# Kernel optimization log

Hardware: AMD Instinct MI355X
Metric: run time of the kernel (lower is better)

The kernel has to match this reference:

```python
import jax, jax.numpy as jnp
import numpy as np

N = 65536          # nodes
E = 1048576        # edges (avg degree 16)
K = 5              # B-spline kernel size per dim (dim=3 -> 125 kernels)
F_IN, F_OUT = 1, 32
GRID = 32          # first sparse_voxel_max_pool: size = 1/32 -> 32^3 voxels
NUM_VOX = GRID ** 3

# enumerate the 2^3 corners of the degree-1 B-spline support
_BITS = np.array([[(b >> d) & 1 for d in range(3)] for b in range(8)], dtype=np.int32)  # [8,3]
_STRIDES = np.array([1, K, K * K], dtype=np.int32)  # kernel index strides per dim


def setup_inputs() -> dict:
    key = jax.random.key(0)
    ks = jax.random.split(key, 7)
    x = jax.random.normal(ks[0], (N, F_IN), dtype=jnp.float32)
    edge_index = jax.random.randint(ks[1], (2, E), 0, N, dtype=jnp.int32)
    pseudo = jax.random.uniform(ks[2], (E, 3), dtype=jnp.float32)   # edge pseudo-coords in [0,1]^3
    pos = jax.random.uniform(ks[3], (N, 3), dtype=jnp.float32)      # node positions in [0,1]^3
    W = jax.random.normal(ks[4], (K ** 3, F_IN, F_OUT), dtype=jnp.float32) * 0.1
    W_root = jax.random.normal(ks[5], (F_IN, F_OUT), dtype=jnp.float32) * 0.1
    bias = jax.random.normal(ks[6], (F_OUT,), dtype=jnp.float32) * 0.1
    return {"x": x, "edge_index": edge_index, "pseudo": pseudo, "pos": pos,
            "W": W, "W_root": W_root, "bias": bias}


def spline_basis(pseudo):
    """Degree-1 open B-spline basis. Returns (weights [E,8], kernel_idx [E,8])."""
    v = pseudo * (K - 1)                                   # [E,3] in [0, K-1]
    i0 = jnp.clip(jnp.floor(v), 0, K - 2)                  # lower knot per dim
    f = v - i0                                             # fractional part
    i0 = i0.astype(jnp.int32)
    bits = jnp.asarray(_BITS)                              # [8,3]
    idx = i0[:, None, :] + bits[None]                      # [E,8,3]
    w = jnp.where(bits[None].astype(bool), f[:, None, :], 1.0 - f[:, None, :])
    B = w.prod(axis=-1)                                    # [E,8]
    kidx = (idx * jnp.asarray(_STRIDES)).sum(axis=-1)      # [E,8] in [0,125)
    return B, kidx


def spline_conv(x, edge_index, pseudo, W, W_root, bias):
    src, dst = edge_index[0], edge_index[1]
    B, kidx = spline_basis(pseudo)                         # [E,8], [E,8]
    xj = x[src]                                            # [E,F_IN] edge-wise gather
    Wg = W[kidx]                                           # [E,8,F_IN,F_OUT]
    msg = jnp.einsum('es,ef,esfo->eo', B, xj, Wg)          # basis-weighted messages [E,F_OUT]
    agg = jax.ops.segment_sum(msg, dst, num_segments=N)    # scatter-add
    deg = jax.ops.segment_sum(jnp.ones((E,), jnp.float32), dst, num_segments=N)
    out = agg / jnp.clip(deg, 1.0)[:, None] + x @ W_root + bias  # mean aggr + root + bias
    return out


def reference(x, edge_index, pseudo, pos, W, W_root, bias):
    h = jax.nn.elu(spline_conv(x, edge_index, pseudo, W, W_root, bias))  # [N,32]
    # sparse voxel max pooling: hash positions to a 32^3 grid, scatter-max features
    vid = jnp.clip(jnp.floor(pos * GRID), 0, GRID - 1).astype(jnp.int32)  # [N,3]
    vidx = vid[:, 0] + GRID * vid[:, 1] + GRID * GRID * vid[:, 2]         # [N]
    pooled = jax.ops.segment_max(h, vidx, num_segments=NUM_VOX)           # [32768,32]
    pooled = jnp.where(jnp.isfinite(pooled), pooled, 0.0)                 # empty voxels -> 0
    return pooled
```

## Files before the change

kernel.cpp:

```cpp
#include <hip/hip_runtime.h>
#include <math.h>

#define F_OUT     32
#define GRID_DIM  32
#define NUM_VOX   (GRID_DIM * GRID_DIM * GRID_DIM)

#define NPB   64
#define NBKT  1024
#define SEB   1024
#define CAP   1344
#define SCS   132
#define DEGS  125

__device__ __forceinline__ unsigned int enc_f32(float f) {
    unsigned int u = __float_as_uint(f);
    return (u & 0x80000000u) ? ~u : (u | 0x80000000u);
}
__device__ __forceinline__ float dec_f32(unsigned int e) {
    return (e & 0x80000000u) ? __uint_as_float(e ^ 0x80000000u)
                             : __uint_as_float(~e);
}

__global__ __launch_bounds__(512) void scatter_kernel(
    const int*   __restrict__ src,
    const int*   __restrict__ dst,
    const float* __restrict__ x,
    const float* __restrict__ pseudo,
    float4* __restrict__ payload,
    unsigned int* __restrict__ cursor,
    int E)
{
    __shared__ unsigned int sHist[NBKT];
    __shared__ unsigned int sCur[NBKT];

    const int t  = threadIdx.x;
    const int e0 = blockIdx.x * SEB;

    for (int i = t; i < NBKT; i += 512) sHist[i] = 0;
    __syncthreads();

    unsigned short dloc[SEB / 512];
    float4 pay[SEB / 512];
    #pragma unroll
    for (int i = 0; i < SEB / 512; ++i) {
        int e = e0 + i * 512 + t;
        if (e < E) {
            int d = dst[e];
            int s = src[e];
            float p0 = pseudo[3 * e], p1 = pseudo[3 * e + 1], p2 = pseudo[3 * e + 2];
            float xj = x[s];
            unsigned int q2 = (unsigned int)(p2 * 65535.0f + 0.5f) & 0xFFFFu;
            unsigned int w  = q2 | ((unsigned int)(d & 63) << 16);
            dloc[i] = (unsigned short)d;
            pay[i]  = make_float4(p0, p1, xj, __uint_as_float(w));
            atomicAdd(&sHist[d >> 6], 1u);
        }
    }
    __syncthreads();

    for (int b = t; b < NBKT; b += 512) {
        unsigned int c = sHist[b];
        sCur[b] = c ? atomicAdd(&cursor[b], c) : 0u;
    }
    __syncthreads();

    #pragma unroll
    for (int i = 0; i < SEB / 512; ++i) {
        int e = e0 + i * 512 + t;
        if (e < E) {
            unsigned int bkt  = (unsigned int)dloc[i] >> 6;
            unsigned int slot = atomicAdd(&sCur[bkt], 1u);
            if (slot < CAP)
                payload[(size_t)bkt * CAP + slot] = pay[i];
        }
    }
}

__device__ __forceinline__ void process_edge(float4 r, float* sC)
{
    float xj = r.z;
    unsigned int w = __float_as_uint(r.w);
    int   rel = (int)((w >> 16) & 63u);
    float p2  = (float)(w & 0xFFFFu) * (1.0f / 65535.0f);

    float v0 = r.x * 4.0f, v1 = r.y * 4.0f, v2 = p2 * 4.0f;
    float i0 = fminf(fmaxf(floorf(v0), 0.0f), 3.0f);
    float i1 = fminf(fmaxf(floorf(v1), 0.0f), 3.0f);
    float i2 = fminf(fmaxf(floorf(v2), 0.0f), 3.0f);
    float f0 = v0 - i0, f1 = v1 - i1, f2 = v2 - i2;
    float g0 = 1.0f - f0, g1 = 1.0f - f1, g2 = 1.0f - f2;
    int k = (int)i0 + 5 * (int)i1 + 25 * (int)i2;

    float w00 = g0 * g1, w10 = f0 * g1, w01 = g0 * f1, w11 = f0 * f1;
    float a2 = xj * g2, b2 = xj * f2;
    float* row = sC + rel * SCS;
    atomicAdd(row + k +  0, w00 * a2);
    atomicAdd(row + k +  1, w10 * a2);
    atomicAdd(row + k +  5, w01 * a2);
    atomicAdd(row + k +  6, w11 * a2);
    atomicAdd(row + k + 25, w00 * b2);
    atomicAdd(row + k + 26, w10 * b2);
    atomicAdd(row + k + 30, w01 * b2);
    atomicAdd(row + k + 31, w11 * b2);
    atomicAdd(row + DEGS, 1.0f);
}

__global__ __launch_bounds__(512) void owner_kernel(
    const float4* __restrict__ payload,
    const unsigned int* __restrict__ cursor,
    const float* __restrict__ W,
    const float* __restrict__ x,
    const float* __restrict__ W_root,
    const float* __restrict__ bias,
    const float* __restrict__ pos,
    unsigned int* __restrict__ pooled,
    int Nn)
{
    __shared__ __align__(16) float sC[NPB * SCS];

    const int t = threadIdx.x;
    const int b = blockIdx.x;

    for (int i = t; i < NPB * SCS / 4; i += 512)
        *(float4*)&sC[i * 4] = make_float4(0.f, 0.f, 0.f, 0.f);
    __syncthreads();

    int cnt = (int)cursor[b];
    if (cnt > CAP) cnt = CAP;
    const float4* slab = payload + (size_t)b * CAP;
    {
        int i = t;
        if (i < cnt) {
            float4 r = slab[i];
            for (i += 512; i < cnt; i += 512) {
                float4 rn = slab[i];
                process_edge(r, sC);
                r = rn;
            }
            process_edge(r, sC);
        }
    }
    __syncthreads();

    const int node = t & 63;
    const int cg   = t >> 6;
    const float* crow = sC + node * SCS;
    float4 acc = make_float4(0.f, 0.f, 0.f, 0.f);
    #pragma unroll 8
    for (int k4 = 0; k4 < 31; ++k4) {
        float4 r = *(const float4*)&crow[k4 * 4];
        const float* wp = W + (k4 * 4) * F_OUT + cg * 4;
        float4 w0 = *(const float4*)(wp);
        float4 w1 = *(const float4*)(wp + F_OUT);
        float4 w2 = *(const float4*)(wp + 2 * F_OUT);
        float4 w3 = *(const float4*)(wp + 3 * F_OUT);
        acc.x += r.x * w0.x + r.y * w1.x + r.z * w2.x + r.w * w3.x;
        acc.y += r.x * w0.y + r.y * w1.y + r.z * w2.y + r.w * w3.y;
        acc.z += r.x * w0.z + r.y * w1.z + r.z * w2.z + r.w * w3.z;
        acc.w += r.x * w0.w + r.y * w1.w + r.z * w2.w + r.w * w3.w;
    }
    {
        float r = crow[124];
        const float* wp = W + 124 * F_OUT + cg * 4;
        acc.x += r * wp[0]; acc.y += r * wp[1];
        acc.z += r * wp[2]; acc.w += r * wp[3];
    }
    float dg = fmaxf(crow[DEGS], 1.0f);
    int   n  = b * NPB + node;
    float xn = (n < Nn) ? x[n] : 0.0f;
    float4 wr = *(const float4*)(W_root + cg * 4);
    float4 bs = *(const float4*)(bias + cg * 4);
    __syncthreads();

    if (n < Nn) {
        float h;
        h = acc.x / dg + xn * wr.x + bs.x; h = h > 0.f ? h : expm1f(h); sC[node * SCS + cg * 4 + 0] = h;
        h = acc.y / dg + xn * wr.y + bs.y; h = h > 0.f ? h : expm1f(h); sC[node * SCS + cg * 4 + 1] = h;
        h = acc.z / dg + xn * wr.z + bs.z; h = h > 0.f ? h : expm1f(h); sC[node * SCS + cg * 4 + 2] = h;
        h = acc.w / dg + xn * wr.w + bs.w; h = h > 0.f ? h : expm1f(h); sC[node * SCS + cg * 4 + 3] = h;
    }
    __syncthreads();

    for (int item = t; item < NPB * F_OUT; item += 512) {
        int nr = item >> 5, o = item & 31;
        int nn = b * NPB + nr;
        if (nn >= Nn) break;
        int vx = min(max((int)floorf(pos[3 * nn + 0] * (float)GRID_DIM), 0), GRID_DIM - 1);
        int vy = min(max((int)floorf(pos[3 * nn + 1] * (float)GRID_DIM), 0), GRID_DIM - 1);
        int vz = min(max((int)floorf(pos[3 * nn + 2] * (float)GRID_DIM), 0), GRID_DIM - 1);
        int vidx = vx + GRID_DIM * vy + GRID_DIM * GRID_DIM * vz;
        atomicMax(&pooled[(size_t)vidx * F_OUT + o], enc_f32(sC[nr * SCS + o]));
    }
}

__global__ __launch_bounds__(256) void finalize_kernel(
    const unsigned int* pooled,
    float* out, int M)
{
    int i = blockIdx.x * blockDim.x + threadIdx.x;
    if (i >= M) return;
    unsigned int u = pooled[i];
    out[i] = (u == 0u) ? 0.0f : dec_f32(u);
}

extern "C" void kernel_launch(void* const* d_in, const int* in_sizes, int n_in,
                              void* d_out, int out_size, void* d_ws, size_t ws_size,
                              hipStream_t stream) {
    const float* x       = (const float*)d_in[0];
    const int*   ei      = (const int*)  d_in[1];
    const float* pseudo  = (const float*)d_in[2];
    const float* pos     = (const float*)d_in[3];
    const float* W       = (const float*)d_in[4];
    const float* W_root  = (const float*)d_in[5];
    const float* bias    = (const float*)d_in[6];

    const int E   = in_sizes[1] / 2;
    const int Nn  = in_sizes[0];
    const int nSB = (E + SEB - 1) / SEB;
    const int nb  = (Nn + NPB - 1) / NPB;

    float4*       payload = (float4*)d_ws;
    unsigned int* cursor  = (unsigned int*)((char*)d_ws + (size_t)NBKT * CAP * sizeof(float4));

    unsigned int* pooled = (unsigned int*)d_out;
    const int M = (out_size < NUM_VOX * F_OUT) ? out_size : NUM_VOX * F_OUT;

    hipMemsetAsync(cursor, 0, NBKT * sizeof(unsigned int), stream);
    hipMemsetAsync(d_out, 0, (size_t)M * sizeof(float), stream);

    scatter_kernel<<<nSB, 512, 0, stream>>>(ei, ei + E, x, pseudo, payload, cursor, E);
    owner_kernel<<<nb, 512, 0, stream>>>(payload, cursor, W, x, W_root, bias, pos,
                                         pooled, Nn);
    finalize_kernel<<<(M + 255) / 256, 256, 0, stream>>>(pooled, (float*)d_out, M);
}
```

Before: 179.7 us.

## Split owner blocks into node halves and pad bucket cursors to separate lines

Each 64-node bucket is now handled by two 256-thread blocks, each owning 32 nodes. Each block reads the whole bucket slab and discards edges whose destination falls in the other half. This doubles the block count and halves the shared accumulator per block, which is meant to raise occupancy and parallelism. The cost is that every payload slab is read twice from global memory. Bucket cursors are also spaced 32 words apart so the global atomics in the scatter kernel do not contend on the same cache lines.

```diff
diff --git a/kernel.cpp b/kernel.cpp
--- a/kernel.cpp
+++ b/kernel.cpp
@@ -11,6 +11,7 @@
 #define CAP   1344
 #define SCS   132
 #define DEGS  125
+#define CSTR  32
 
 __device__ __forceinline__ unsigned int enc_f32(float f) {
     unsigned int u = __float_as_uint(f);
@@ -60,7 +61,7 @@
 
     for (int b = t; b < NBKT; b += 512) {
         unsigned int c = sHist[b];
-        sCur[b] = c ? atomicAdd(&cursor[b], c) : 0u;
+        sCur[b] = c ? atomicAdd(&cursor[(size_t)b * CSTR], c) : 0u;
     }
     __syncthreads();
 
@@ -76,12 +77,14 @@
     }
 }
 
-__device__ __forceinline__ void process_edge(float4 r, float* sC)
-{
+__device__ __forceinline__ void process_edge(float4 r, float* sC, int half)
+{
+    unsigned int w = __float_as_uint(r.w);
+    int rel6 = (int)((w >> 16) & 63u);
+    if ((rel6 >> 5) != half) return;
+
     float xj = r.z;
-    unsigned int w = __float_as_uint(r.w);
-    int   rel = (int)((w >> 16) & 63u);
-    float p2  = (float)(w & 0xFFFFu) * (1.0f / 65535.0f);
+    float p2 = (float)(w & 0xFFFFu) * (1.0f / 65535.0f);
 
     float v0 = r.x * 4.0f, v1 = r.y * 4.0f, v2 = p2 * 4.0f;
     float i0 = fminf(fmaxf(floorf(v0), 0.0f), 3.0f);
@@ -93,7 +96,7 @@
 
     float w00 = g0 * g1, w10 = f0 * g1, w01 = g0 * f1, w11 = f0 * f1;
     float a2 = xj * g2, b2 = xj * f2;
-    float* row = sC + rel * SCS;
+    float* row = sC + (rel6 & 31) * SCS;
     atomicAdd(row + k +  0, w00 * a2);
     atomicAdd(row + k +  1, w10 * a2);
     atomicAdd(row + k +  5, w01 * a2);
@@ -105,7 +108,7 @@
     atomicAdd(row + DEGS, 1.0f);
 }
 
-__global__ __launch_bounds__(512) void owner_kernel(
+__global__ __launch_bounds__(256) void owner_kernel(
     const float4* __restrict__ payload,
     const unsigned int* __restrict__ cursor,
     const float* __restrict__ W,
@@ -116,34 +119,36 @@
     unsigned int* __restrict__ pooled,
     int Nn)
 {
-    __shared__ __align__(16) float sC[NPB * SCS];
-
-    const int t = threadIdx.x;
-    const int b = blockIdx.x;
-
-    for (int i = t; i < NPB * SCS / 4; i += 512)
+    __shared__ __align__(16) float sC[32 * SCS];
+
+    const int t    = threadIdx.x;
+    const int bp   = blockIdx.x;
+    const int b    = bp >> 1;
+    const int half = bp & 1;
+
+    for (int i = t; i < 32 * SCS / 4; i += 256)
         *(float4*)&sC[i * 4] = make_float4(0.f, 0.f, 0.f, 0.f);
     __syncthreads();
 
-    int cnt = (int)cursor[b];
+    int cnt = (int)cursor[(size_t)b * CSTR];
     if (cnt > CAP) cnt = CAP;
     const float4* slab = payload + (size_t)b * CAP;
     {
         int i = t;
         if (i < cnt) {
             float4 r = slab[i];
-            for (i += 512; i < cnt; i += 512) {
+            for (i += 256; i < cnt; i += 256) {
                 float4 rn = slab[i];
-                process_edge(r, sC);
+                process_edge(r, sC, half);
                 r = rn;
             }
-            process_edge(r, sC);
+            process_edge(r, sC, half);
         }
     }
     __syncthreads();
 
-    const int node = t & 63;
-    const int cg   = t >> 6;
+    const int node = t & 31;
+    const int cg   = t >> 5;
     const float* crow = sC + node * SCS;
     float4 acc = make_float4(0.f, 0.f, 0.f, 0.f);
     #pragma unroll 8
@@ -166,7 +171,7 @@
         acc.z += r * wp[2]; acc.w += r * wp[3];
     }
     float dg = fmaxf(crow[DEGS], 1.0f);
-    int   n  = b * NPB + node;
+    int   n  = b * NPB + half * 32 + node;
     float xn = (n < Nn) ? x[n] : 0.0f;
     float4 wr = *(const float4*)(W_root + cg * 4);
     float4 bs = *(const float4*)(bias + cg * 4);
@@ -181,9 +186,9 @@
     }
     __syncthreads();
 
-    for (int item = t; item < NPB * F_OUT; item += 512) {
+    for (int item = t; item < 32 * F_OUT; item += 256) {
         int nr = item >> 5, o = item & 31;
-        int nn = b * NPB + nr;
+        int nn = b * NPB + half * 32 + nr;
         if (nn >= Nn) break;
         int vx = min(max((int)floorf(pos[3 * nn + 0] * (float)GRID_DIM), 0), GRID_DIM - 1);
         int vy = min(max((int)floorf(pos[3 * nn + 1] * (float)GRID_DIM), 0), GRID_DIM - 1);
@@ -217,7 +222,7 @@
     const int E   = in_sizes[1] / 2;
     const int Nn  = in_sizes[0];
     const int nSB = (E + SEB - 1) / SEB;
-    const int nb  = (Nn + NPB - 1) / NPB;
+    const int nb  = 2 * ((Nn + NPB - 1) / NPB);
 
     float4*       payload = (float4*)d_ws;
     unsigned int* cursor  = (unsigned int*)((char*)d_ws + (size_t)NBKT * CAP * sizeof(float4));
@@ -225,11 +230,11 @@
     unsigned int* pooled = (unsigned int*)d_out;
     const int M = (out_size < NUM_VOX * F_OUT) ? out_size : NUM_VOX * F_OUT;
 
-    hipMemsetAsync(cursor, 0, NBKT * sizeof(unsigned int), stream);
+    hipMemsetAsync(cursor, 0, (size_t)NBKT * CSTR * sizeof(unsigned int), stream);
     hipMemsetAsync(d_out, 0, (size_t)M * sizeof(float), stream);
 
     scatter_kernel<<<nSB, 512, 0, stream>>>(ei, ei + E, x, pseudo, payload, cursor, E);
-    owner_kernel<<<nb, 512, 0, stream>>>(payload, cursor, W, x, W_root, bias, pos,
+    owner_kernel<<<nb, 256, 0, stream>>>(payload, cursor, W, x, W_root, bias, pos,
                                          pooled, Nn);
     finalize_kernel<<<(M + 255) / 256, 256, 0, stream>>>(pooled, (float*)d_out, M);
 }
```

Measured after the change: 186.0 us. 1.03x slower.
